# Kernel optimization log

Measured on AMD Instinct MI355X. Metric: run time of the kernel, lower is better.

Reference implementation:

```python
import jax, jax.numpy as jnp
import numpy as np

NUM_GRAPHS = 512
N_NODES = 500000
C = 256
R = 16

def setup_inputs() -> dict:
    key = jax.random.key(0)
    k1, k2, k3, k4 = jax.random.split(key, 4)
    x = jax.random.normal(k1, (N_NODES, C), dtype=jnp.float32)
    batch = jnp.sort(jax.random.randint(k2, (N_NODES,), 0, NUM_GRAPHS, dtype=jnp.int64))
    # Linear weights (torch stores [out,in]; we use [in,out] for x @ W)
    W1 = jax.random.normal(k3, (C, C // R), dtype=jnp.float32) * (1.0 / np.sqrt(C))
    W2 = jax.random.normal(k4, (C // R, C), dtype=jnp.float32) * (1.0 / np.sqrt(C // R))
    return {"x": x, "batch": batch, "W1": W1, "W2": W2}

def reference(x, batch, W1, W2):
    batch = batch.astype(jnp.int32)
    # segment mean pool: [G, C]
    seg_sum = jax.ops.segment_sum(x, batch, num_segments=NUM_GRAPHS)
    counts = jax.ops.segment_sum(jnp.ones((x.shape[0],), x.dtype), batch, num_segments=NUM_GRAPHS)
    mean_pool = seg_sum / jnp.maximum(counts, 1.0)[:, None]
    # squeeze-excite MLP: Linear -> ReLU -> Linear -> Sigmoid
    scale = jax.nn.sigmoid(jax.nn.relu(mean_pool @ W1) @ W2)  # [G, C]
    # repeat_interleave(scale, bincount(batch)) on sorted batch == gather by batch
    return x * scale[batch]
```

## Files before the change

kernel.cpp:

```cpp
#include <hip/hip_runtime.h>

#define NCH 256
#define HID 16
#define NBLK 256
#define SREG 40

typedef __attribute__((ext_vector_type(4))) float f32x4;
typedef __attribute__((ext_vector_type(4))) unsigned int u32x4;

__device__ __forceinline__ f32x4 ldrow(const float* __restrict__ x, int r, size_t coff) {
    return *reinterpret_cast<const f32x4*>(x + (size_t)r * NCH + coff);
}

__device__ __forceinline__ void strow(float* __restrict__ out, int r, size_t coff, f32x4 v) {
    __builtin_nontemporal_store(v, reinterpret_cast<f32x4*>(out + (size_t)r * NCH + coff));
}

__device__ __forceinline__ u32x4 packrow(f32x4 a, f32x4 b) {
    u32x4 ua = __builtin_bit_cast(u32x4, a) + 0x8000u;
    u32x4 ub = __builtin_bit_cast(u32x4, b) + 0x8000u;
    return (ua & 0xffff0000u) | (ub >> 16);
}
__device__ __forceinline__ f32x4 unhi(u32x4 p) { return __builtin_bit_cast(f32x4, p & 0xffff0000u); }
__device__ __forceinline__ f32x4 unlo(u32x4 p) { return __builtin_bit_cast(f32x4, p << 16); }

__device__ __forceinline__ void se_mlp(const float* __restrict__ W1,
                                       const float* __restrict__ W2,
                                       float (&s_part)[8][NCH], int cnt,
                                       float* __restrict__ s_vec,
                                       float (&s_hp)[HID][17], float (&s_h)[HID],
                                       int tid)
{
    if (tid < NCH) {
        float m = 0.f;
        #pragma unroll
        for (int i = 0; i < 8; ++i) m += s_part[i][tid];
        m *= (cnt > 0) ? (1.0f / (float)cnt) : 1.0f;
        s_vec[tid] = m;
    }
    __syncthreads();
    if (tid < NCH) {
        const int j = tid >> 4, sub = tid & 15;
        float hp = 0.f;
        #pragma unroll
        for (int i = 0; i < 16; ++i) { int c = sub * 16 + i; hp += s_vec[c] * W1[c * HID + j]; }
        s_hp[j][sub] = hp;
    }
    __syncthreads();
    if (tid < HID) {
        float h = 0.f;
        #pragma unroll
        for (int i = 0; i < 16; ++i) h += s_hp[tid][i];
        s_h[tid] = fmaxf(h, 0.f);
    }
    __syncthreads();
    if (tid < NCH) {
        float sc = 0.f;
        #pragma unroll
        for (int j = 0; j < HID; ++j) sc += s_h[j] * W2[j * NCH + tid];
        s_vec[tid] = 1.0f / (1.0f + __expf(-sc));
    }
}

__global__ __launch_bounds__(512, 1) void graph_se_kernel(
    const float* __restrict__ x,
    const int* __restrict__ batch,
    const float* __restrict__ W1,
    const float* __restrict__ W2,
    float* __restrict__ out,
    int n)
{
    const int b   = blockIdx.x;
    const int tid = threadIdx.x;

    __shared__ unsigned int s_stash[128][NCH];
    __shared__ int   s_bnd[4];
    __shared__ float s_part[8][NCH];
    __shared__ float s_vecA[NCH];
    __shared__ float s_vecB[NCH];
    __shared__ float s_hp[HID][17];
    __shared__ float s_h[HID];

    if (tid < 4) {
        int v = (tid < 2) ? (b + tid) : (NBLK + b + (tid - 2));
        int lo = 0, hi = n;
        while (lo < hi) { int mid = (lo + hi) >> 1; if (batch[mid] < v) lo = mid + 1; else hi = mid; }
        s_bnd[tid] = lo;
    }
    __syncthreads();
    const int loA = s_bnd[0], hiA = s_bnd[1];
    const int loB = s_bnd[2], hiB = s_bnd[3];

    const int rg = tid >> 6;
    const int c4 = tid & 63;
    const size_t coff = (size_t)c4 * 4;

    f32x4 st[SREG];

    const int base2 = loA + 8 * SREG;
    const int tailA = base2 + 256;

    {
        f32x4 acc = (f32x4)(0.f);
        #pragma unroll
        for (int j = 0; j < SREG; ++j) {
            int r0 = loA + rg + 8 * j;
            if (r0 < hiA) { st[j] = ldrow(x, r0, coff); acc += st[j]; }
        }
        #pragma unroll 2
        for (int k = 0; k < 16; ++k) {
            int i  = rg + 8 * k;
            int r0 = base2 + i, r1 = r0 + 128;
            f32x4 v0 = (f32x4)(0.f), v1 = (f32x4)(0.f);
            if (r0 < hiA) { v0 = ldrow(x, r0, coff); acc += v0; }
            if (r1 < hiA) { v1 = ldrow(x, r1, coff); acc += v1; }
            *reinterpret_cast<u32x4*>(&s_stash[i][c4 * 4]) = packrow(v0, v1);
        }
        int r = tailA + rg;
        for (; r + 24 < hiA; r += 32) {
            f32x4 v0 = ldrow(x, r     , coff);
            f32x4 v1 = ldrow(x, r +  8, coff);
            f32x4 v2 = ldrow(x, r + 16, coff);
            f32x4 v3 = ldrow(x, r + 24, coff);
            acc += (v0 + v1) + (v2 + v3);
        }
        for (; r < hiA; r += 8) acc += ldrow(x, r, coff);
        *reinterpret_cast<f32x4*>(&s_part[rg][c4 * 4]) = acc;
    }
    __syncthreads();

    se_mlp(W1, W2, s_part, hiA - loA, s_vecA, s_hp, s_h, tid);
    __syncthreads();

    const f32x4 scvA = *reinterpret_cast<const f32x4*>(&s_vecA[c4 * 4]);

    #pragma unroll
    for (int j = 0; j < SREG; ++j) {
        int rA = loA + rg + 8 * j;
        if (rA < hiA) strow(out, rA, coff, st[j] * scvA);
    }

    {
        f32x4 accB = (f32x4)(0.f);
        #pragma unroll
        for (int j = 0; j < SREG; ++j) {
            int rB = loB + rg + 8 * j;
            if (rB < hiB) { st[j] = ldrow(x, rB, coff); accB += st[j]; }
        }
        int r = loB + 8 * SREG + rg;
        for (; r + 24 < hiB; r += 32) {
            f32x4 v0 = ldrow(x, r     , coff);
            f32x4 v1 = ldrow(x, r +  8, coff);
            f32x4 v2 = ldrow(x, r + 16, coff);
            f32x4 v3 = ldrow(x, r + 24, coff);
            accB += (v0 + v1) + (v2 + v3);
        }
        for (; r < hiB; r += 8) accB += ldrow(x, r, coff);
        *reinterpret_cast<f32x4*>(&s_part[rg][c4 * 4]) = accB;
    }
    __syncthreads();

    se_mlp(W1, W2, s_part, hiB - loB, s_vecB, s_hp, s_h, tid);
    __syncthreads();

    {
        const f32x4 scvB = *reinterpret_cast<const f32x4*>(&s_vecB[c4 * 4]);
        #pragma unroll
        for (int j = 0; j < SREG; ++j) {
            int rB = loB + rg + 8 * j;
            if (rB < hiB) strow(out, rB, coff, st[j] * scvB);
        }
        #pragma unroll 2
        for (int k = 0; k < 16; ++k) {
            int i  = rg + 8 * k;
            u32x4 p = *reinterpret_cast<const u32x4*>(&s_stash[i][c4 * 4]);
            int r0 = base2 + i, r1 = r0 + 128;
            if (r0 < hiA) strow(out, r0, coff, unhi(p) * scvA);
            if (r1 < hiA) strow(out, r1, coff, unlo(p) * scvA);
        }
        int r = tailA + rg;
        for (; r + 24 < hiA; r += 32) {
            f32x4 v0 = ldrow(x, r     , coff);
            f32x4 v1 = ldrow(x, r +  8, coff);
            f32x4 v2 = ldrow(x, r + 16, coff);
            f32x4 v3 = ldrow(x, r + 24, coff);
            strow(out, r     , coff, v0 * scvA);
            strow(out, r +  8, coff, v1 * scvA);
            strow(out, r + 16, coff, v2 * scvA);
            strow(out, r + 24, coff, v3 * scvA);
        }
        for (; r < hiA; r += 8) strow(out, r, coff, ldrow(x, r, coff) * scvA);
        r = loB + 8 * SREG + rg;
        for (; r + 24 < hiB; r += 32) {
            f32x4 v0 = ldrow(x, r     , coff);
            f32x4 v1 = ldrow(x, r +  8, coff);
            f32x4 v2 = ldrow(x, r + 16, coff);
            f32x4 v3 = ldrow(x, r + 24, coff);
            strow(out, r     , coff, v0 * scvB);
            strow(out, r +  8, coff, v1 * scvB);
            strow(out, r + 16, coff, v2 * scvB);
            strow(out, r + 24, coff, v3 * scvB);
        }
        for (; r < hiB; r += 8) strow(out, r, coff, ldrow(x, r, coff) * scvB);
    }
}

extern "C" void kernel_launch(void* const* d_in, const int* in_sizes, int n_in,
                              void* d_out, int out_size, void* d_ws, size_t ws_size,
                              hipStream_t stream) {
    const float* x     = (const float*)d_in[0];
    const int*   batch = (const int*)d_in[1];
    const float* W1    = (const float*)d_in[2];
    const float* W2    = (const float*)d_in[3];
    float*       out   = (float*)d_out;
    const int n = in_sizes[1];

    hipLaunchKernelGGL(graph_se_kernel, dim3(NBLK), dim3(512), 0, stream,
                       x, batch, W1, W2, out, n);
}
```

Before: 278.3 us.

## Double block threads and overlap graph A writeback with graph B reduction

Each block now runs 1024 threads in 16 row groups instead of 512 threads in 8, and the register stash shrinks from 40 to 16 rows per thread. After graph A's scale is computed, half the groups write out A's LDS-stashed rows and tail. Meanwhile the other half start loading and reducing graph B, and the first half then pick up part of B's head rows. The goal is to hide the latency between the two per-graph phases and give more memory parallelism. The cost is fewer rows held in registers, so more tail rows must be re-read from global memory, plus extra branching between the two groups.

```diff
diff --git a/kernel.cpp b/kernel.cpp
--- a/kernel.cpp
+++ b/kernel.cpp
@@ -3,7 +3,7 @@
 #define NCH 256
 #define HID 16
 #define NBLK 256
-#define SREG 40
+#define SREG 16
 
 typedef __attribute__((ext_vector_type(4))) float f32x4;
 typedef __attribute__((ext_vector_type(4))) unsigned int u32x4;
@@ -26,7 +26,7 @@
 
 __device__ __forceinline__ void se_mlp(const float* __restrict__ W1,
                                        const float* __restrict__ W2,
-                                       float (&s_part)[8][NCH], int cnt,
+                                       float (&s_part)[16][NCH], int cnt,
                                        float* __restrict__ s_vec,
                                        float (&s_hp)[HID][17], float (&s_h)[HID],
                                        int tid)
@@ -34,7 +34,7 @@
     if (tid < NCH) {
         float m = 0.f;
         #pragma unroll
-        for (int i = 0; i < 8; ++i) m += s_part[i][tid];
+        for (int i = 0; i < 16; ++i) m += s_part[i][tid];
         m *= (cnt > 0) ? (1.0f / (float)cnt) : 1.0f;
         s_vec[tid] = m;
     }
@@ -62,7 +62,7 @@
     }
 }
 
-__global__ __launch_bounds__(512, 1) void graph_se_kernel(
+__global__ __launch_bounds__(1024, 4) void graph_se_kernel(
     const float* __restrict__ x,
     const int* __restrict__ batch,
     const float* __restrict__ W1,
@@ -75,7 +75,7 @@
 
     __shared__ unsigned int s_stash[128][NCH];
     __shared__ int   s_bnd[4];
-    __shared__ float s_part[8][NCH];
+    __shared__ float s_part[16][NCH];
     __shared__ float s_vecA[NCH];
     __shared__ float s_vecB[NCH];
     __shared__ float s_hp[HID][17];
@@ -97,34 +97,35 @@
 
     f32x4 st[SREG];
 
-    const int base2 = loA + 8 * SREG;
-    const int tailA = base2 + 256;
+    const int ldsA  = loA + 16 * SREG;
+    const int tailA = ldsA + 256;
+    const int tailB = loB + 256;
 
     {
         f32x4 acc = (f32x4)(0.f);
         #pragma unroll
         for (int j = 0; j < SREG; ++j) {
-            int r0 = loA + rg + 8 * j;
+            int r0 = loA + rg + 16 * j;
             if (r0 < hiA) { st[j] = ldrow(x, r0, coff); acc += st[j]; }
         }
         #pragma unroll 2
-        for (int k = 0; k < 16; ++k) {
-            int i  = rg + 8 * k;
-            int r0 = base2 + i, r1 = r0 + 128;
+        for (int k = 0; k < 8; ++k) {
+            int i  = rg + 16 * k;
+            int r0 = ldsA + i, r1 = r0 + 128;
             f32x4 v0 = (f32x4)(0.f), v1 = (f32x4)(0.f);
             if (r0 < hiA) { v0 = ldrow(x, r0, coff); acc += v0; }
             if (r1 < hiA) { v1 = ldrow(x, r1, coff); acc += v1; }
             *reinterpret_cast<u32x4*>(&s_stash[i][c4 * 4]) = packrow(v0, v1);
         }
         int r = tailA + rg;
-        for (; r + 24 < hiA; r += 32) {
-            f32x4 v0 = ldrow(x, r     , coff);
-            f32x4 v1 = ldrow(x, r +  8, coff);
-            f32x4 v2 = ldrow(x, r + 16, coff);
-            f32x4 v3 = ldrow(x, r + 24, coff);
+        for (; r + 48 < hiA; r += 64) {
+            f32x4 v0 = ldrow(x, r     , coff);
+            f32x4 v1 = ldrow(x, r + 16, coff);
+            f32x4 v2 = ldrow(x, r + 32, coff);
+            f32x4 v3 = ldrow(x, r + 48, coff);
             acc += (v0 + v1) + (v2 + v3);
         }
-        for (; r < hiA; r += 8) acc += ldrow(x, r, coff);
+        for (; r < hiA; r += 16) acc += ldrow(x, r, coff);
         *reinterpret_cast<f32x4*>(&s_part[rg][c4 * 4]) = acc;
     }
     __syncthreads();
@@ -136,45 +137,15 @@
 
     #pragma unroll
     for (int j = 0; j < SREG; ++j) {
-        int rA = loA + rg + 8 * j;
+        int rA = loA + rg + 16 * j;
         if (rA < hiA) strow(out, rA, coff, st[j] * scvA);
     }
-
-    {
-        f32x4 accB = (f32x4)(0.f);
-        #pragma unroll
-        for (int j = 0; j < SREG; ++j) {
-            int rB = loB + rg + 8 * j;
-            if (rB < hiB) { st[j] = ldrow(x, rB, coff); accB += st[j]; }
-        }
-        int r = loB + 8 * SREG + rg;
-        for (; r + 24 < hiB; r += 32) {
-            f32x4 v0 = ldrow(x, r     , coff);
-            f32x4 v1 = ldrow(x, r +  8, coff);
-            f32x4 v2 = ldrow(x, r + 16, coff);
-            f32x4 v3 = ldrow(x, r + 24, coff);
-            accB += (v0 + v1) + (v2 + v3);
-        }
-        for (; r < hiB; r += 8) accB += ldrow(x, r, coff);
-        *reinterpret_cast<f32x4*>(&s_part[rg][c4 * 4]) = accB;
-    }
-    __syncthreads();
-
-    se_mlp(W1, W2, s_part, hiB - loB, s_vecB, s_hp, s_h, tid);
-    __syncthreads();
-
-    {
-        const f32x4 scvB = *reinterpret_cast<const f32x4*>(&s_vecB[c4 * 4]);
-        #pragma unroll
-        for (int j = 0; j < SREG; ++j) {
-            int rB = loB + rg + 8 * j;
-            if (rB < hiB) strow(out, rB, coff, st[j] * scvB);
-        }
+    if (rg < 8) {
         #pragma unroll 2
         for (int k = 0; k < 16; ++k) {
             int i  = rg + 8 * k;
             u32x4 p = *reinterpret_cast<const u32x4*>(&s_stash[i][c4 * 4]);
-            int r0 = base2 + i, r1 = r0 + 128;
+            int r0 = ldsA + i, r1 = r0 + 128;
             if (r0 < hiA) strow(out, r0, coff, unhi(p) * scvA);
             if (r1 < hiA) strow(out, r1, coff, unlo(p) * scvA);
         }
@@ -190,18 +161,65 @@
             strow(out, r + 24, coff, v3 * scvA);
         }
         for (; r < hiA; r += 8) strow(out, r, coff, ldrow(x, r, coff) * scvA);
-        r = loB + 8 * SREG + rg;
+        f32x4 accB = (f32x4)(0.f);
+        #pragma unroll
+        for (int j = 0; j < SREG; ++j) {
+            int rB = loB + 128 + rg + 8 * j;
+            if (rB < hiB) { st[j] = ldrow(x, rB, coff); accB += st[j]; }
+        }
+        *reinterpret_cast<f32x4*>(&s_part[rg][c4 * 4]) = accB;
+    } else {
+        const int gid = rg - 8;
+        f32x4 accB = (f32x4)(0.f);
+        #pragma unroll
+        for (int j = 0; j < SREG; ++j) {
+            int rB = loB + gid + 8 * j;
+            if (rB < hiB) { st[j] = ldrow(x, rB, coff); accB += st[j]; }
+        }
+        int r = tailB + gid;
         for (; r + 24 < hiB; r += 32) {
             f32x4 v0 = ldrow(x, r     , coff);
             f32x4 v1 = ldrow(x, r +  8, coff);
             f32x4 v2 = ldrow(x, r + 16, coff);
             f32x4 v3 = ldrow(x, r + 24, coff);
+            accB += (v0 + v1) + (v2 + v3);
+        }
+        for (; r < hiB; r += 8) accB += ldrow(x, r, coff);
+        *reinterpret_cast<f32x4*>(&s_part[rg][c4 * 4]) = accB;
+    }
+    __syncthreads();
+
+    se_mlp(W1, W2, s_part, hiB - loB, s_vecB, s_hp, s_h, tid);
+    __syncthreads();
+
+    {
+        const f32x4 scvB = *reinterpret_cast<const f32x4*>(&s_vecB[c4 * 4]);
+        if (rg < 8) {
+            #pragma unroll
+            for (int j = 0; j < SREG; ++j) {
+                int rB = loB + 128 + rg + 8 * j;
+                if (rB < hiB) strow(out, rB, coff, st[j] * scvB);
+            }
+        } else {
+            const int gid = rg - 8;
+            #pragma unroll
+            for (int j = 0; j < SREG; ++j) {
+                int rB = loB + gid + 8 * j;
+                if (rB < hiB) strow(out, rB, coff, st[j] * scvB);
+            }
+        }
+        int r = tailB + rg;
+        for (; r + 48 < hiB; r += 64) {
+            f32x4 v0 = ldrow(x, r     , coff);
+            f32x4 v1 = ldrow(x, r + 16, coff);
+            f32x4 v2 = ldrow(x, r + 32, coff);
+            f32x4 v3 = ldrow(x, r + 48, coff);
             strow(out, r     , coff, v0 * scvB);
-            strow(out, r +  8, coff, v1 * scvB);
-            strow(out, r + 16, coff, v2 * scvB);
-            strow(out, r + 24, coff, v3 * scvB);
-        }
-        for (; r < hiB; r += 8) strow(out, r, coff, ldrow(x, r, coff) * scvB);
+            strow(out, r + 16, coff, v1 * scvB);
+            strow(out, r + 32, coff, v2 * scvB);
+            strow(out, r + 48, coff, v3 * scvB);
+        }
+        for (; r < hiB; r += 16) strow(out, r, coff, ldrow(x, r, coff) * scvB);
     }
 }
 
@@ -215,6 +233,6 @@
     float*       out   = (float*)d_out;
     const int n = in_sizes[1];
 
-    hipLaunchKernelGGL(graph_se_kernel, dim3(NBLK), dim3(512), 0, stream,
+    hipLaunchKernelGGL(graph_se_kernel, dim3(NBLK), dim3(1024), 0, stream,
                        x, batch, W1, W2, out, n);
 }
```

Measured after the change: 244.1 us (median of 2 runs). 12.3% less time.
